# Performance work log

Measured on AMD Instinct MI355X. Metric: run time of the kernel, lower is better.

The kernel has to match this reference:

```python
import jax, jax.numpy as jnp
import numpy as np

B, D_IN, H, N_LAYERS, D_OUT = 262144, 8, 128, 3, 1


def setup_inputs() -> dict:
    key = jax.random.key(0)
    ks = jax.random.split(key, 18)
    rn = lambda k, shape, fan: (jax.random.normal(k, shape, jnp.float32) / np.sqrt(fan))
    return {
        "x": jax.random.normal(ks[0], (B, D_IN), jnp.float32),
        "Sw_w": rn(ks[1], (D_IN, H), D_IN),
        "Sw_b": rn(ks[2], (H,), D_IN),
        "Uz": rn(ks[3], (N_LAYERS, D_IN, H), D_IN),
        "Wsz_w": rn(ks[4], (N_LAYERS, H, H), H),
        "Wsz_b": rn(ks[5], (N_LAYERS, H), H),
        "Ug": rn(ks[6], (N_LAYERS, D_IN, H), D_IN),
        "Wsg_w": rn(ks[7], (N_LAYERS, H, H), H),
        "Wsg_b": rn(ks[8], (N_LAYERS, H), H),
        "Ur": rn(ks[9], (N_LAYERS, D_IN, H), D_IN),
        "Wsr_w": rn(ks[10], (N_LAYERS, H, H), H),
        "Wsr_b": rn(ks[11], (N_LAYERS, H), H),
        "Uh": rn(ks[12], (N_LAYERS, D_IN, H), D_IN),
        "Wsh_w": rn(ks[13], (N_LAYERS, H, H), H),
        "Wsh_b": rn(ks[14], (N_LAYERS, H), H),
        "Wf_w": rn(ks[15], (H, D_OUT), H),
        "Wf_b": rn(ks[16], (D_OUT,), H),
    }


def reference(x, Sw_w, Sw_b, Uz, Wsz_w, Wsz_b, Ug, Wsg_w, Wsg_b,
              Ur, Wsr_w, Wsr_b, Uh, Wsh_w, Wsh_b, Wf_w, Wf_b):
    # x: [B, D_in]; S: [B, H]
    S = x @ Sw_w + Sw_b
    n = Uz.shape[0]
    for i in range(n):  # small fixed layer count
        S = jax.nn.sigmoid(S)
        Z = jax.nn.sigmoid(x @ Uz[i] + S @ Wsz_w[i] + Wsz_b[i])
        G = jax.nn.sigmoid(x @ Ug[i] + S @ Wsg_w[i] + Wsg_b[i])
        R = jax.nn.sigmoid(x @ Ur[i] + S @ Wsr_w[i] + Wsr_b[i])
        H_ = jnp.tanh(x @ Uh[i] + (S * R) @ Wsh_w[i] + Wsh_b[i])
        S = (1.0 - G) * H_ + Z * S
    return S @ Wf_w + Wf_b  # [B, D_out]
```

## Files before the change

kernel.cpp:

```cpp
#include <hip/hip_runtime.h>

typedef __bf16 bf16_t;
typedef __bf16 bf16x2 __attribute__((ext_vector_type(2)));
typedef __bf16 bf16x8 __attribute__((ext_vector_type(8)));
typedef float f32x4 __attribute__((ext_vector_type(4)));

#define NL 3
#define HD 128
#define ROWS 64
#define STR 136
#define THREADS 512
#define BATCH 262144
#define NBLK (BATCH / ROWS)

#define SW_OFF 0
#define U_OFF  4096
#define W_OFF  53248
#define WS_ELEMS 249856

#define MFMA(a, b, c) __builtin_amdgcn_mfma_f32_16x16x32_bf16((a), (b), (c), 0, 0, 0)

#define LOG2E 1.4426950408889634f
__device__ __forceinline__ float sigm(float v) {
    return __builtin_amdgcn_rcpf(1.f + __builtin_amdgcn_exp2f(-LOG2E * v));
}
__device__ __forceinline__ float sigmn(float v) {
    return __builtin_amdgcn_rcpf(1.f + __builtin_amdgcn_exp2f(LOG2E * v));
}
__device__ __forceinline__ float tanh_f(float v) {
    return 1.f - 2.f * __builtin_amdgcn_rcpf(__builtin_amdgcn_exp2f((2.f * LOG2E) * v) + 1.f);
}

__global__ void dgm_prep(const float* __restrict__ SwW,
                         const float* __restrict__ Uz, const float* __restrict__ Wz,
                         const float* __restrict__ Ug, const float* __restrict__ Wg,
                         const float* __restrict__ Ur, const float* __restrict__ Wr,
                         const float* __restrict__ Uh, const float* __restrict__ Wh,
                         bf16_t* __restrict__ ws) {
    int idx = blockIdx.x * 256 + threadIdx.x;
    if (idx >= WS_ELEMS) return;
    const float* Us[4] = {Uz, Ug, Ur, Uh};
    const float* Wm[4] = {Wz, Wg, Wr, Wh};
    if (idx < U_OFF) {
        int ct = idx >> 9, rem = idx & 511, lane = rem >> 3, j = rem & 7;
        int q = lane >> 4, mm = lane & 15;
        int k = q * 8 + j, n = ct * 16 + mm;
        ws[idx] = (k < 8) ? (bf16_t)SwW[k * HD + n] : (bf16_t)0.f;
    } else if (idx < W_OFF) {
        int t = idx - U_OFF;
        int lg = t >> 12, r2 = t & 4095;
        int l = lg >> 2, g = lg & 3;
        int ct = r2 >> 9, rem = r2 & 511, lane = rem >> 3, j = rem & 7;
        int q = lane >> 4, mm = lane & 15;
        int k = q * 8 + j, n = ct * 16 + mm;
        ws[idx] = (k < 8) ? (bf16_t)Us[g][(l * 8 + k) * HD + n] : (bf16_t)0.f;
    } else {
        int t = idx - W_OFF;
        int lg = t >> 14, r2 = t & 16383;
        int l = lg >> 2, g = lg & 3;
        int ct = r2 >> 11, kc = (r2 >> 9) & 3, rem = r2 & 511, lane = rem >> 3, j = rem & 7;
        int q = lane >> 4, mm = lane & 15;
        int k = kc * 32 + q * 8 + j, n = ct * 16 + mm;
        ws[idx] = (bf16_t)Wm[g][(l * HD + k) * HD + n];
    }
}

__global__ __launch_bounds__(THREADS, 4) void dgm_main(
    const float* __restrict__ x,
    const float* __restrict__ Swb,
    const float* __restrict__ Bz, const float* __restrict__ Bg,
    const float* __restrict__ Br, const float* __restrict__ Bh,
    const float* __restrict__ WfW, const float* __restrict__ WfB,
    const bf16_t* __restrict__ ws,
    float* __restrict__ out) {
    __shared__ __align__(16) bf16_t s_sig[2][ROWS * STR];
    __shared__ __align__(16) bf16_t s_r[ROWS * STR];
    __shared__ float red[ROWS];

    const int tid = threadIdx.x;
    const int lane = tid & 63;
    const int ct = tid >> 6;
    const int m = lane & 15, q = lane >> 4;
    const int rb = blockIdx.x * ROWS;
    const int c = ct * 16 + m;
    const int fragoff = (ct * 64 + lane) * 8;

    if (tid < ROWS) red[tid] = 0.f;

    {
        int r = tid >> 3, j = tid & 7;
        bf16_t xv = (bf16_t)x[(size_t)(rb + r) * 8 + j];
        s_sig[0][r * STR + 128 + j] = xv;
        s_sig[1][r * STR + 128 + j] = xv;
        s_r[r * STR + 128 + j] = xv;
    }
    __syncthreads();

    bf16x2 svp[4][2];

    {
        const float swb = Swb[c];
        bf16x8 fSw = *(const bf16x8*)(ws + SW_OFF + fragoff);
#pragma unroll
        for (int rt = 0; rt < 4; rt++) {
            bf16x8 a = *(const bf16x8*)(&s_sig[0][(rt * 16 + m) * STR + 128]);
            f32x4 acc = {0.f, 0.f, 0.f, 0.f};
            acc = MFMA(a, fSw, acc);
#pragma unroll
            for (int i = 0; i < 4; i++) {
                bf16_t s0 = (bf16_t)sigm(acc[i] + swb);
                svp[rt][i >> 1][i & 1] = s0;
                s_sig[0][(rt * 16 + q * 4 + i) * STR + c] = s0;
            }
        }
    }
    __syncthreads();

#pragma unroll 1
    for (int l = 0; l < NL; l++) {
        const int cur = l & 1, nxt = cur ^ 1;
        const bf16_t* wb = ws + W_OFF + (size_t)l * 4 * 16384;
        const bf16_t* ub = ws + U_OFF + (size_t)l * 4 * 4096;

        {
            bf16x8 fU = *(const bf16x8*)(ub + 2 * 4096 + fragoff);
            bf16x8 fW[4];
#pragma unroll
            for (int kc = 0; kc < 4; kc++)
                fW[kc] = *(const bf16x8*)(wb + 2 * 16384 + (ct * 4 + kc) * 512 + lane * 8);
            const float br = Br[l * HD + c];
#pragma unroll
            for (int rt = 0; rt < 4; rt++) {
                const bf16_t* abase = &s_sig[cur][(rt * 16 + m) * STR];
                f32x4 aR = {0.f, 0.f, 0.f, 0.f};
#pragma unroll
                for (int kc = 0; kc < 4; kc++) {
                    bf16x8 a = *(const bf16x8*)(abase + kc * 32 + q * 8);
                    aR = MFMA(a, fW[kc], aR);
                }
                {
                    bf16x8 a = *(const bf16x8*)(abase + 128);
                    aR = MFMA(a, fU, aR);
                }
#pragma unroll
                for (int i = 0; i < 4; i++) {
                    int r = rt * 16 + q * 4 + i;
                    float sb = (float)svp[rt][i >> 1][i & 1];
                    s_r[r * STR + c] = (bf16_t)(sigm(aR[i] + br) * sb);
                }
            }
        }
        __syncthreads();

        bf16x2 t1p[4][2];
        bf16x2 ogp[4][2];

        {
            bf16x8 fUz = *(const bf16x8*)(ub + 0 * 4096 + fragoff);
            bf16x8 fUg = *(const bf16x8*)(ub + 1 * 4096 + fragoff);
            bf16x8 fWz[4], fWg[4];
#pragma unroll
            for (int kc = 0; kc < 4; kc++) {
                fWz[kc] = *(const bf16x8*)(wb + 0 * 16384 + (ct * 4 + kc) * 512 + lane * 8);
                fWg[kc] = *(const bf16x8*)(wb + 1 * 16384 + (ct * 4 + kc) * 512 + lane * 8);
            }
            const float bz = Bz[l * HD + c], bg = Bg[l * HD + c];
#pragma unroll
            for (int rt = 0; rt < 4; rt++) {
                const bf16_t* abase = &s_sig[cur][(rt * 16 + m) * STR];
                f32x4 aZ = {0.f, 0.f, 0.f, 0.f}, aG = {0.f, 0.f, 0.f, 0.f};
#pragma unroll
                for (int kc = 0; kc < 4; kc++) {
                    bf16x8 a = *(const bf16x8*)(abase + kc * 32 + q * 8);
                    aZ = MFMA(a, fWz[kc], aZ);
                    aG = MFMA(a, fWg[kc], aG);
                }
                {
                    bf16x8 a = *(const bf16x8*)(abase + 128);
                    aZ = MFMA(a, fUz, aZ);
                    aG = MFMA(a, fUg, aG);
                }
#pragma unroll
                for (int i = 0; i < 4; i++) {
                    float sb = (float)svp[rt][i >> 1][i & 1];
                    t1p[rt][i >> 1][i & 1] = (bf16_t)(sigm(aZ[i] + bz) * sb);
                    ogp[rt][i >> 1][i & 1] = (bf16_t)sigmn(aG[i] + bg);
                }
            }
        }

        {
            bf16x8 fU = *(const bf16x8*)(ub + 3 * 4096 + fragoff);
            bf16x8 fW[4];
#pragma unroll
            for (int kc = 0; kc < 4; kc++)
                fW[kc] = *(const bf16x8*)(wb + 3 * 16384 + (ct * 4 + kc) * 512 + lane * 8);
            const float bh = Bh[l * HD + c];
            const bool last = (l == NL - 1);
            const float wfc = WfW[c];
#pragma unroll
            for (int rt = 0; rt < 4; rt++) {
                const bf16_t* abase = &s_r[(rt * 16 + m) * STR];
                f32x4 aH = {0.f, 0.f, 0.f, 0.f};
#pragma unroll
                for (int kc = 0; kc < 4; kc++) {
                    bf16x8 a = *(const bf16x8*)(abase + kc * 32 + q * 8);
                    aH = MFMA(a, fW[kc], aH);
                }
                {
                    bf16x8 a = *(const bf16x8*)(abase + 128);
                    aH = MFMA(a, fU, aH);
                }
#pragma unroll
                for (int i = 0; i < 4; i++) {
                    int r = rt * 16 + q * 4 + i;
                    float hh = tanh_f(aH[i] + bh);
                    float sn = (float)ogp[rt][i >> 1][i & 1] * hh + (float)t1p[rt][i >> 1][i & 1];
                    if (last) {
                        float p = sn * wfc;
                        p += __shfl_xor(p, 1);
                        p += __shfl_xor(p, 2);
                        p += __shfl_xor(p, 4);
                        p += __shfl_xor(p, 8);
                        if (m == 0) atomicAdd(&red[r], p);
                    } else {
                        bf16_t s2 = (bf16_t)sigm(sn);
                        svp[rt][i >> 1][i & 1] = s2;
                        s_sig[nxt][r * STR + c] = s2;
                    }
                }
            }
        }
        __syncthreads();
    }

    if (tid < ROWS) out[rb + tid] = red[tid] + WfB[0];
}

extern "C" void kernel_launch(void* const* d_in, const int* in_sizes, int n_in,
                              void* d_out, int out_size, void* d_ws, size_t ws_size,
                              hipStream_t stream) {
    const float* x   = (const float*)d_in[0];
    const float* SwW = (const float*)d_in[1];
    const float* Swb = (const float*)d_in[2];
    const float* Uz  = (const float*)d_in[3];
    const float* Wz  = (const float*)d_in[4];
    const float* Bz  = (const float*)d_in[5];
    const float* Ug  = (const float*)d_in[6];
    const float* Wg  = (const float*)d_in[7];
    const float* Bg  = (const float*)d_in[8];
    const float* Ur  = (const float*)d_in[9];
    const float* Wr  = (const float*)d_in[10];
    const float* Br  = (const float*)d_in[11];
    const float* Uh  = (const float*)d_in[12];
    const float* Wh  = (const float*)d_in[13];
    const float* Bh  = (const float*)d_in[14];
    const float* WfW = (const float*)d_in[15];
    const float* WfB = (const float*)d_in[16];
    bf16_t* ws = (bf16_t*)d_ws;
    float* out = (float*)d_out;

    if (ws_size < (size_t)WS_ELEMS * sizeof(bf16_t)) return;

    dgm_prep<<<(WS_ELEMS + 255) / 256, 256, 0, stream>>>(SwW, Uz, Wz, Ug, Wg, Ur, Wr, Uh, Wh, ws);
    dgm_main<<<NBLK, THREADS, 0, stream>>>(x, Swb, Bz, Bg, Br, Bh, WfW, WfB, ws, out);
}
```

Before: 298.3 us.

## Prefetch next-stage weight fragments and split MFMA phases from activation epilogues

Restructures each layer so that the weight fragments for the next GEMM stage (Z/G, then H, then the next layer's R) are loaded from global memory while the current stage's MFMAs and activations run. It also separates each stage into a pure MFMA phase that keeps all four row-tile accumulators live, followed by a transcendental epilogue, so matrix and vector work can interleave. The aim is to hide global-load latency and keep the MFMA units busier. The cost is higher VGPR pressure from extra live fragments and accumulators, which could lower occupancy.

Result: slower. 319.5 us (+7.1%).

```diff
diff --git a/kernel.cpp b/kernel.cpp
--- a/kernel.cpp
+++ b/kernel.cpp
@@ -84,6 +84,7 @@
     const int rb = blockIdx.x * ROWS;
     const int c = ct * 16 + m;
     const int fragoff = (ct * 64 + lane) * 8;
+    const int wfragoff = (ct * 4) * 512 + lane * 8;
 
     if (tid < ROWS) red[tid] = 0.f;
 
@@ -98,6 +99,16 @@
 
     bf16x2 svp[4][2];
 
+    bf16x8 fUr, fWr[4];
+    {
+        const bf16_t* ub0 = ws + U_OFF;
+        const bf16_t* wb0 = ws + W_OFF;
+        fUr = *(const bf16x8*)(ub0 + 2 * 4096 + fragoff);
+#pragma unroll
+        for (int kc = 0; kc < 4; kc++)
+            fWr[kc] = *(const bf16x8*)(wb0 + 2 * 16384 + wfragoff + kc * 512);
+    }
+
     {
         const float swb = Swb[c];
         bf16x8 fSw = *(const bf16x8*)(ws + SW_OFF + fragoff);
@@ -122,99 +133,123 @@
         const bf16_t* wb = ws + W_OFF + (size_t)l * 4 * 16384;
         const bf16_t* ub = ws + U_OFF + (size_t)l * 4 * 4096;
 
+        f32x4 aR[4];
+#pragma unroll
+        for (int rt = 0; rt < 4; rt++) {
+            const bf16_t* abase = &s_sig[cur][(rt * 16 + m) * STR];
+            f32x4 acc = {0.f, 0.f, 0.f, 0.f};
+#pragma unroll
+            for (int kc = 0; kc < 4; kc++) {
+                bf16x8 a = *(const bf16x8*)(abase + kc * 32 + q * 8);
+                acc = MFMA(a, fWr[kc], acc);
+            }
+            {
+                bf16x8 a = *(const bf16x8*)(abase + 128);
+                acc = MFMA(a, fUr, acc);
+            }
+            aR[rt] = acc;
+        }
+
+        bf16x8 fUz = *(const bf16x8*)(ub + 0 * 4096 + fragoff);
+        bf16x8 fUg = *(const bf16x8*)(ub + 1 * 4096 + fragoff);
+        bf16x8 fWz[4], fWg[4];
+#pragma unroll
+        for (int kc = 0; kc < 4; kc++) {
+            fWz[kc] = *(const bf16x8*)(wb + 0 * 16384 + wfragoff + kc * 512);
+            fWg[kc] = *(const bf16x8*)(wb + 1 * 16384 + wfragoff + kc * 512);
+        }
+
         {
-            bf16x8 fU = *(const bf16x8*)(ub + 2 * 4096 + fragoff);
-            bf16x8 fW[4];
-#pragma unroll
-            for (int kc = 0; kc < 4; kc++)
-                fW[kc] = *(const bf16x8*)(wb + 2 * 16384 + (ct * 4 + kc) * 512 + lane * 8);
             const float br = Br[l * HD + c];
 #pragma unroll
-            for (int rt = 0; rt < 4; rt++) {
-                const bf16_t* abase = &s_sig[cur][(rt * 16 + m) * STR];
-                f32x4 aR = {0.f, 0.f, 0.f, 0.f};
-#pragma unroll
-                for (int kc = 0; kc < 4; kc++) {
-                    bf16x8 a = *(const bf16x8*)(abase + kc * 32 + q * 8);
-                    aR = MFMA(a, fW[kc], aR);
-                }
-                {
-                    bf16x8 a = *(const bf16x8*)(abase + 128);
-                    aR = MFMA(a, fU, aR);
-                }
+            for (int rt = 0; rt < 4; rt++)
 #pragma unroll
                 for (int i = 0; i < 4; i++) {
                     int r = rt * 16 + q * 4 + i;
                     float sb = (float)svp[rt][i >> 1][i & 1];
-                    s_r[r * STR + c] = (bf16_t)(sigm(aR[i] + br) * sb);
+                    s_r[r * STR + c] = (bf16_t)(sigm(aR[rt][i] + br) * sb);
                 }
-            }
         }
         __syncthreads();
 
         bf16x2 t1p[4][2];
         bf16x2 ogp[4][2];
 
+        f32x4 aZ[4], aG[4];
+#pragma unroll
+        for (int rt = 0; rt < 4; rt++) {
+            const bf16_t* abase = &s_sig[cur][(rt * 16 + m) * STR];
+            f32x4 az = {0.f, 0.f, 0.f, 0.f}, ag = {0.f, 0.f, 0.f, 0.f};
+#pragma unroll
+            for (int kc = 0; kc < 4; kc++) {
+                bf16x8 a = *(const bf16x8*)(abase + kc * 32 + q * 8);
+                az = MFMA(a, fWz[kc], az);
+                ag = MFMA(a, fWg[kc], ag);
+            }
+            {
+                bf16x8 a = *(const bf16x8*)(abase + 128);
+                az = MFMA(a, fUz, az);
+                ag = MFMA(a, fUg, ag);
+            }
+            aZ[rt] = az;
+            aG[rt] = ag;
+        }
+
+        bf16x8 fUh = *(const bf16x8*)(ub + 3 * 4096 + fragoff);
+        bf16x8 fWh[4];
+#pragma unroll
+        for (int kc = 0; kc < 4; kc++)
+            fWh[kc] = *(const bf16x8*)(wb + 3 * 16384 + wfragoff + kc * 512);
+
         {
-            bf16x8 fUz = *(const bf16x8*)(ub + 0 * 4096 + fragoff);
-            bf16x8 fUg = *(const bf16x8*)(ub + 1 * 4096 + fragoff);
-            bf16x8 fWz[4], fWg[4];
-#pragma unroll
-            for (int kc = 0; kc < 4; kc++) {
-                fWz[kc] = *(const bf16x8*)(wb + 0 * 16384 + (ct * 4 + kc) * 512 + lane * 8);
-                fWg[kc] = *(const bf16x8*)(wb + 1 * 16384 + (ct * 4 + kc) * 512 + lane * 8);
-            }
             const float bz = Bz[l * HD + c], bg = Bg[l * HD + c];
 #pragma unroll
-            for (int rt = 0; rt < 4; rt++) {
-                const bf16_t* abase = &s_sig[cur][(rt * 16 + m) * STR];
-                f32x4 aZ = {0.f, 0.f, 0.f, 0.f}, aG = {0.f, 0.f, 0.f, 0.f};
-#pragma unroll
-                for (int kc = 0; kc < 4; kc++) {
-                    bf16x8 a = *(const bf16x8*)(abase + kc * 32 + q * 8);
-                    aZ = MFMA(a, fWz[kc], aZ);
-                    aG = MFMA(a, fWg[kc], aG);
-                }
-                {
-                    bf16x8 a = *(const bf16x8*)(abase + 128);
-                    aZ = MFMA(a, fUz, aZ);
-                    aG = MFMA(a, fUg, aG);
-                }
+            for (int rt = 0; rt < 4; rt++)
 #pragma unroll
                 for (int i = 0; i < 4; i++) {
                     float sb = (float)svp[rt][i >> 1][i & 1];
-                    t1p[rt][i >> 1][i & 1] = (bf16_t)(sigm(aZ[i] + bz) * sb);
-                    ogp[rt][i >> 1][i & 1] = (bf16_t)sigmn(aG[i] + bg);
+                    t1p[rt][i >> 1][i & 1] = (bf16_t)(sigm(aZ[rt][i] + bz) * sb);
+                    ogp[rt][i >> 1][i & 1] = (bf16_t)sigmn(aG[rt][i] + bg);
                 }
-            }
+        }
+
+        f32x4 aH[4];
+#pragma unroll
+        for (int rt = 0; rt < 4; rt++) {
+            const bf16_t* abase = &s_r[(rt * 16 + m) * STR];
+            f32x4 acc = {0.f, 0.f, 0.f, 0.f};
+#pragma unroll
+            for (int kc = 0; kc < 4; kc++) {
+                bf16x8 a = *(const bf16x8*)(abase + kc * 32 + q * 8);
+                acc = MFMA(a, fWh[kc], acc);
+            }
+            {
+                bf16x8 a = *(const bf16x8*)(abase + 128);
+                acc = MFMA(a, fUh, acc);
+            }
+            aH[rt] = acc;
         }
 
         {
-            bf16x8 fU = *(const bf16x8*)(ub + 3 * 4096 + fragoff);
-            bf16x8 fW[4];
+            int ln = (l < NL - 1) ? (l + 1) : l;
+            const bf16_t* ubn = ws + U_OFF + (size_t)ln * 4 * 4096;
+            const bf16_t* wbn = ws + W_OFF + (size_t)ln * 4 * 16384;
+            fUr = *(const bf16x8*)(ubn + 2 * 4096 + fragoff);
 #pragma unroll
             for (int kc = 0; kc < 4; kc++)
-                fW[kc] = *(const bf16x8*)(wb + 3 * 16384 + (ct * 4 + kc) * 512 + lane * 8);
+                fWr[kc] = *(const bf16x8*)(wbn + 2 * 16384 + wfragoff + kc * 512);
+        }
+
+        {
             const float bh = Bh[l * HD + c];
             const bool last = (l == NL - 1);
             const float wfc = WfW[c];
 #pragma unroll
-            for (int rt = 0; rt < 4; rt++) {
-                const bf16_t* abase = &s_r[(rt * 16 + m) * STR];
-                f32x4 aH = {0.f, 0.f, 0.f, 0.f};
-#pragma unroll
-                for (int kc = 0; kc < 4; kc++) {
-                    bf16x8 a = *(const bf16x8*)(abase + kc * 32 + q * 8);
-                    aH = MFMA(a, fW[kc], aH);
-                }
-                {
-                    bf16x8 a = *(const bf16x8*)(abase + 128);
-                    aH = MFMA(a, fU, aH);
-                }
+            for (int rt = 0; rt < 4; rt++)
 #pragma unroll
                 for (int i = 0; i < 4; i++) {
                     int r = rt * 16 + q * 4 + i;
-                    float hh = tanh_f(aH[i] + bh);
+                    float hh = tanh_f(aH[rt][i] + bh);
                     float sn = (float)ogp[rt][i >> 1][i & 1] * hh + (float)t1p[rt][i >> 1][i & 1];
                     if (last) {
                         float p = sn * wfc;
@@ -229,7 +264,6 @@
                         s_sig[nxt][r * STR + c] = s2;
                     }
                 }
-            }
         }
         __syncthreads();
     }
```
